# Optimization experiments

Measured on AMD Instinct MI355X. Metric: run time of the kernel, lower is better.

The kernel has to match this reference:

```python
import jax, jax.numpy as jnp
import numpy as np
import math

FANO_LINES = [(0,1,2),(0,3,4),(0,6,5),(1,3,5),(1,4,6),(2,3,6),(2,5,4)]
WINDOW = 16

def fano_mask(T: int) -> jnp.ndarray:
    """[7,T,T] bool mask: head h attends to j if (j%7 in line_h and j<=i) or i-WINDOW<=j<=i."""
    membership = np.zeros((7, 7), dtype=bool)
    for h, line in enumerate(FANO_LINES):
        membership[h, list(line)] = True
    j = np.arange(T)
    fano = membership[:, j % 7]                      # [7,T]
    i = j[:, None]
    causal = (j[None, :] <= i)                       # [T,T]
    local = causal & (j[None, :] >= i - WINDOW)      # [T,T]
    mask = (fano[:, None, :] & causal[None]) | local[None]
    return jnp.asarray(mask)

def setup_inputs() -> dict:
    key = jax.random.key(0)
    ks = jax.random.split(key, 5)
    B, T, D = 1, 4096, 896
    s = 1.0 / math.sqrt(D)
    return {
        "x":  jax.random.normal(ks[0], (B, T, D), dtype=jnp.float32),
        "Wq": jax.random.normal(ks[1], (D, D), dtype=jnp.float32) * s,
        "Wk": jax.random.normal(ks[2], (D, D), dtype=jnp.float32) * s,
        "Wv": jax.random.normal(ks[3], (D, D), dtype=jnp.float32) * s,
        "Wo": jax.random.normal(ks[4], (D, D), dtype=jnp.float32) * s,
    }

def reference(x, Wq, Wk, Wv, Wo):
    B, T, D = x.shape
    H = 7
    hd = D // H
    # torch Linear: x @ W.T
    q = (x @ Wq.T).reshape(B, T, H, hd)
    k = (x @ Wk.T).reshape(B, T, H, hd)
    v = (x @ Wv.T).reshape(B, T, H, hd)
    scale = 1.0 / math.sqrt(hd)
    scores = jnp.einsum('bthc,bshc->bhts', q, k) * scale   # [B,7,T,T]
    mask = fano_mask(T)                                    # [7,T,T]
    neg = jnp.asarray(-jnp.inf, dtype=scores.dtype)
    scores = jnp.where(mask[None], scores, neg)
    attn = jax.nn.softmax(scores, axis=-1)
    out = jnp.einsum('bhts,bshc->bthc', attn, v).reshape(B, T, D)
    return out @ Wo.T
```

## Files before the change

### kernel.cpp

```cpp
#include <hip/hip_runtime.h>
#include <stdint.h>

typedef unsigned short ushort_t;
typedef __bf16 bf16x8 __attribute__((ext_vector_type(8)));
typedef float f32x4 __attribute__((ext_vector_type(4)));

#define T_SEQ 4096
#define D_MODEL 896
#define NSPLIT 4

#define LSK 136
#define LSV 72
#define LSP 72

__constant__ int d_LINEMASK[7] = {0x07, 0x19, 0x61, 0x2A, 0x52, 0x4C, 0x34};
__constant__ int d_R[7][3] = {{0,1,2},{0,3,4},{0,5,6},{1,3,5},{1,4,6},{2,3,6},{2,4,5}};

__device__ inline unsigned f2bf(float f) {
    unsigned x = __float_as_uint(f);
    return (x + 0x7fffu + ((x >> 16) & 1u)) >> 16;
}
__device__ inline float lo_f(unsigned x) { return __uint_as_float(x << 16); }
__device__ inline float hi_f(unsigned x) { return __uint_as_float(x & 0xFFFF0000u); }

__global__ __launch_bounds__(256)
void cvt5(const float* __restrict__ x,  const float* __restrict__ wq,
          const float* __restrict__ wk, const float* __restrict__ wv,
          const float* __restrict__ wo,
          ushort_t* __restrict__ xb,  ushort_t* __restrict__ wqb,
          ushort_t* __restrict__ wkb, ushort_t* __restrict__ wvb,
          ushort_t* __restrict__ wob) {
    const int ten = blockIdx.y;
    const float* s = (ten == 0) ? x : (ten == 1) ? wq : (ten == 2) ? wk
                   : (ten == 3) ? wv : wo;
    ushort_t* d = (ten == 0) ? xb : (ten == 1) ? wqb : (ten == 2) ? wkb
                : (ten == 3) ? wvb : wob;
    const int n8 = ((ten == 0) ? T_SEQ * D_MODEL : D_MODEL * D_MODEL) >> 3;
    for (int i = blockIdx.x * 256 + threadIdx.x; i < n8; i += gridDim.x * 256) {
        float4 a = ((const float4*)s)[2 * i];
        float4 b = ((const float4*)s)[2 * i + 1];
        uint4 u;
        u.x = f2bf(a.x) | (f2bf(a.y) << 16);
        u.y = f2bf(a.z) | (f2bf(a.w) << 16);
        u.z = f2bf(b.x) | (f2bf(b.y) << 16);
        u.w = f2bf(b.z) | (f2bf(b.w) << 16);
        ((uint4*)d)[i] = u;
    }
}

__device__ __forceinline__ void async_cp16(const void* g, void* l) {
    __builtin_amdgcn_global_load_lds(
        (__attribute__((address_space(1))) void*)g,
        (__attribute__((address_space(3))) void*)l,
        16, 0, 0);
}

template <bool C32>
__global__ __launch_bounds__(256)
void gemm_nt_dma(const ushort_t* __restrict__ A,
                 const ushort_t* __restrict__ B0,
                 const ushort_t* __restrict__ B1,
                 const ushort_t* __restrict__ B2,
                 void* __restrict__ C0,
                 void* __restrict__ C1,
                 void* __restrict__ C2) {
    const int z = blockIdx.z;
    const ushort_t* B = (z == 0) ? B0 : (z == 1) ? B1 : B2;
    void* C = (z == 0) ? C0 : (z == 1) ? C1 : C2;

    const int K = D_MODEL, N = D_MODEL;
    const int i0 = blockIdx.x * 128;
    const int n0 = blockIdx.y * 128;

    __shared__ __align__(16) ushort_t As[128 * 32];
    __shared__ __align__(16) ushort_t Bs[128 * 32];

    const int t = threadIdx.x;
    const int w = t >> 6, lane = t & 63;
    const int wm = (w >> 1) * 64, wn = (w & 1) * 64;
    const int lr = lane & 15, lq = lane >> 4;

    const int srow = w * 16 + (lane >> 2);
    const int scol = (lane & 3) * 8;
    const ushort_t* gA0 = A + (size_t)(i0 + srow) * K + scol;
    const ushort_t* gA1 = A + (size_t)(i0 + 64 + srow) * K + scol;
    const ushort_t* gB0 = B + (size_t)(n0 + srow) * K + scol;
    const ushort_t* gB1 = B + (size_t)(n0 + 64 + srow) * K + scol;
    ushort_t* lA0 = &As[(w * 16) * 32];
    ushort_t* lA1 = &As[(64 + w * 16) * 32];
    ushort_t* lB0 = &Bs[(w * 16) * 32];
    ushort_t* lB1 = &Bs[(64 + w * 16) * 32];

    f32x4 acc[4][4];
#pragma unroll
    for (int a = 0; a < 4; a++)
#pragma unroll
        for (int b = 0; b < 4; b++) acc[a][b] = (f32x4){0.f, 0.f, 0.f, 0.f};

    for (int k0 = 0; k0 < K; k0 += 32) {
        __syncthreads();
        async_cp16(gA0 + k0, lA0);
        async_cp16(gA1 + k0, lA1);
        async_cp16(gB0 + k0, lB0);
        async_cp16(gB1 + k0, lB1);
        __builtin_amdgcn_s_waitcnt(0);
        __syncthreads();

        bf16x8 af[4], bfr[4];
#pragma unroll
        for (int mi = 0; mi < 4; mi++)
            af[mi] = *(const bf16x8*)&As[(wm + mi * 16 + lr) * 32 + lq * 8];
#pragma unroll
        for (int ni = 0; ni < 4; ni++)
            bfr[ni] = *(const bf16x8*)&Bs[(wn + ni * 16 + lr) * 32 + lq * 8];
#pragma unroll
        for (int mi = 0; mi < 4; mi++)
#pragma unroll
            for (int ni = 0; ni < 4; ni++)
                acc[mi][ni] = __builtin_amdgcn_mfma_f32_16x16x32_bf16(
                    af[mi], bfr[ni], acc[mi][ni], 0, 0, 0);
    }

    if (C32) {
        float* Cf = (float*)C;
#pragma unroll
        for (int mi = 0; mi < 4; mi++)
#pragma unroll
            for (int ni = 0; ni < 4; ni++)
#pragma unroll
                for (int r = 0; r < 4; r++) {
                    int row = i0 + wm + mi * 16 + lq * 4 + r;
                    int col = n0 + wn + ni * 16 + lr;
                    Cf[(size_t)row * N + col] = acc[mi][ni][r];
                }
    } else {
        ushort_t* Cb = (ushort_t*)C;
#pragma unroll
        for (int mi = 0; mi < 4; mi++)
#pragma unroll
            for (int ni = 0; ni < 4; ni++)
#pragma unroll
                for (int r = 0; r < 4; r++) {
                    int row = i0 + wm + mi * 16 + lq * 4 + r;
                    int col = n0 + wn + ni * 16 + lr;
                    Cb[(size_t)row * N + col] = (ushort_t)f2bf(acc[mi][ni][r]);
                }
    }
}

__device__ inline void vt_scatter8(ushort_t* vtcol, uint4 vv) {
    vtcol[0 * LSV] = (ushort_t)(vv.x & 0xFFFFu);
    vtcol[1 * LSV] = (ushort_t)(vv.x >> 16);
    vtcol[2 * LSV] = (ushort_t)(vv.y & 0xFFFFu);
    vtcol[3 * LSV] = (ushort_t)(vv.y >> 16);
    vtcol[4 * LSV] = (ushort_t)(vv.z & 0xFFFFu);
    vtcol[5 * LSV] = (ushort_t)(vv.z >> 16);
    vtcol[6 * LSV] = (ushort_t)(vv.w & 0xFFFFu);
    vtcol[7 * LSV] = (ushort_t)(vv.w >> 16);
}

__device__ inline int jof(int p, int r0, int r1, int r2) {
    int g = p / 3, rs = p - 3 * g;
    return 7 * g + ((rs == 0) ? r0 : (rs == 1) ? r1 : r2);
}

__device__ __forceinline__ void issue_kv(const ushort_t* __restrict__ Kb,
                                         const ushort_t* __restrict__ Vb,
                                         int j, int h, int dim0,
                                         uint4 kreg[4], uint4 vreg[4]) {
    if (j >= 0 && j < T_SEQ) {
        const ushort_t* kp = Kb + (size_t)j * D_MODEL + h * 128 + dim0;
        const ushort_t* vp = Vb + (size_t)j * D_MODEL + h * 128 + dim0;
#pragma unroll
        for (int v = 0; v < 4; v++) {
            kreg[v] = *(const uint4*)(kp + v * 8);
            vreg[v] = *(const uint4*)(vp + v * 8);
        }
    } else {
        uint4 zz = {0u, 0u, 0u, 0u};
#pragma unroll
        for (int v = 0; v < 4; v++) { kreg[v] = zz; vreg[v] = zz; }
    }
}

__device__ __forceinline__ void write_kv(ushort_t* Ks, ushort_t* Vt,
                                         int kk, int dim0,
                                         const uint4 kreg[4], const uint4 vreg[4]) {
#pragma unroll
    for (int v = 0; v < 4; v++) {
        *(uint4*)&Ks[kk * LSK + dim0 + v * 8] = kreg[v];
        vt_scatter8(&Vt[(dim0 + v * 8) * LSV + kk], vreg[v]);
    }
}

__global__ __launch_bounds__(256, 3)
void fano_attn_split(const ushort_t* __restrict__ Qb,
                     const ushort_t* __restrict__ Kb,
                     const ushort_t* __restrict__ Vb,
                     ushort_t* __restrict__ Opart,
                     float* __restrict__ Lm) {
    const int h = blockIdx.y;
    const int sp = blockIdx.z;
    const int tile = (int)gridDim.x - 1 - (int)blockIdx.x;
    const int i0 = tile * 64;
    const int t = threadIdx.x;
    const int w = t >> 6, lane = t & 63;
    const int lr = lane & 15, quad = lane >> 4;
    const int iw0 = i0 + w * 16;

    __shared__ __align__(16) ushort_t Ks[64 * LSK];
    __shared__ __align__(16) ushort_t Vt[128 * LSV];
    __shared__ __align__(16) ushort_t Ps[64 * LSP];

    const int lm = d_LINEMASK[h];
    const int r0 = d_R[h][0], r1 = d_R[h][1], r2 = d_R[h][2];
    const float scale = 0.08838834764831845f;

    bf16x8 qf[4];
    {
        const ushort_t* qrow = Qb + (size_t)(iw0 + lr) * D_MODEL + h * 128;
#pragma unroll
        for (int f = 0; f < 4; f++)
            qf[f] = *(const bf16x8*)(qrow + f * 32 + quad * 8);
    }

    f32x4 O[8];
#pragma unroll
    for (int dt = 0; dt < 8; dt++) O[dt] = (f32x4){0.f, 0.f, 0.f, 0.f};
    float m[4] = {-1e30f, -1e30f, -1e30f, -1e30f};
    float l[4] = {0.f, 0.f, 0.f, 0.f};

    const int imax = i0 + 63;
    const int ncomp = (imax - r0) / 7 + (imax - r1) / 7 + (imax - r2) / 7 + 3;
    const int nch = (ncomp + 63) >> 6;
    const int ntot = nch + 2;
    const int cstart = (sp * ntot) / NSPLIT;
    const int cend = ((sp + 1) * ntot) / NSPLIT;

    auto chunk_j = [&](int cc) -> int {
        if (cc >= nch) {
            const int jbase = (cc == nch) ? i0 - 16 : i0 + 48;
            return jbase + lane;
        }
        return jof(cc * 64 + lane, r0, r1, r2);
    };

    uint4 kreg[4], vreg[4];
    if (cstart < cend)
        issue_kv(Kb, Vb, chunk_j(cstart), h, w * 32, kreg, vreg);

    for (int cc = cstart; cc < cend; cc++) {
        const bool band = (cc >= nch);
        const int jbase = (cc == nch) ? i0 - 16 : i0 + 48;

        __syncthreads();
        write_kv(Ks, Vt, lane, w * 32, kreg, vreg);
        __syncthreads();

        if (cc + 1 < cend)
            issue_kv(Kb, Vb, chunk_j(cc + 1), h, w * 32, kreg, vreg);

        {
            int jmin = band ? jbase : jof(cc * 64, r0, r1, r2);
            if (jmin > iw0 + 15) continue;
        }

        f32x4 S[4];
#pragma unroll
        for (int tn = 0; tn < 4; tn++) S[tn] = (f32x4){0.f, 0.f, 0.f, 0.f};
#pragma unroll
        for (int f = 0; f < 4; f++) {
            bf16x8 kf[4];
#pragma unroll
            for (int tn = 0; tn < 4; tn++)
                kf[tn] = *(const bf16x8*)&Ks[(tn * 16 + lr) * LSK + f * 32 + quad * 8];
#pragma unroll
            for (int tn = 0; tn < 4; tn++)
                S[tn] = __builtin_amdgcn_mfma_f32_16x16x32_bf16(qf[f], kf[tn], S[tn], 0, 0, 0);
        }

#pragma unroll
        for (int tn = 0; tn < 4; tn++) {
            int j;
            bool okl = true;
            if (band) {
                j = jbase + tn * 16 + lr;
                int jm = ((j % 7) + 7) % 7;
                okl = (j >= 0) && !((lm >> jm) & 1);
            } else {
                j = jof(cc * 64 + tn * 16 + lr, r0, r1, r2);
            }
#pragma unroll
            for (int r = 0; r < 4; r++) {
                int ir = iw0 + quad * 4 + r;
                bool ok = okl && (j <= ir) && (!band || j >= ir - 16);
                S[tn][r] = ok ? S[tn][r] * scale : -1e30f;
            }
        }

        float a4[4], pvv[4][4];
#pragma unroll
        for (int r = 0; r < 4; r++) {
            float cm = fmaxf(fmaxf(S[0][r], S[1][r]), fmaxf(S[2][r], S[3][r]));
            cm = fmaxf(cm, __shfl_xor(cm, 1));
            cm = fmaxf(cm, __shfl_xor(cm, 2));
            cm = fmaxf(cm, __shfl_xor(cm, 4));
            cm = fmaxf(cm, __shfl_xor(cm, 8));
            float mn = fmaxf(fmaxf(m[r], cm), -60.f);
            a4[r] = __expf(m[r] - mn);
            m[r] = mn;
            float rs_ = 0.f;
#pragma unroll
            for (int tn = 0; tn < 4; tn++) {
                pvv[tn][r] = __expf(S[tn][r] - mn);
                rs_ += pvv[tn][r];
            }
            rs_ += __shfl_xor(rs_, 1);
            rs_ += __shfl_xor(rs_, 2);
            rs_ += __shfl_xor(rs_, 4);
            rs_ += __shfl_xor(rs_, 8);
            l[r] = l[r] * a4[r] + rs_;
            ushort_t* pp = &Ps[(w * 16 + quad * 4 + r) * LSP + lr];
            pp[0]  = (ushort_t)f2bf(pvv[0][r]);
            pp[16] = (ushort_t)f2bf(pvv[1][r]);
            pp[32] = (ushort_t)f2bf(pvv[2][r]);
            pp[48] = (ushort_t)f2bf(pvv[3][r]);
        }
#pragma unroll
        for (int dt = 0; dt < 8; dt++)
#pragma unroll
            for (int r = 0; r < 4; r++) O[dt][r] *= a4[r];

        bf16x8 pf0 = *(const bf16x8*)&Ps[(w * 16 + lr) * LSP + quad * 8];
        bf16x8 pf1 = *(const bf16x8*)&Ps[(w * 16 + lr) * LSP + 32 + quad * 8];
#pragma unroll
        for (int dt = 0; dt < 8; dt++) {
            bf16x8 v0 = *(const bf16x8*)&Vt[(dt * 16 + lr) * LSV + quad * 8];
            bf16x8 v1 = *(const bf16x8*)&Vt[(dt * 16 + lr) * LSV + 32 + quad * 8];
            O[dt] = __builtin_amdgcn_mfma_f32_16x16x32_bf16(pf0, v0, O[dt], 0, 0, 0);
            O[dt] = __builtin_amdgcn_mfma_f32_16x16x32_bf16(pf1, v1, O[dt], 0, 0, 0);
        }
    }

    const size_t pbase = ((size_t)sp * 7 + h) * T_SEQ;
#pragma unroll
    for (int dt = 0; dt < 8; dt++)
#pragma unroll
        for (int r = 0; r < 4; r++) {
            int row = iw0 + quad * 4 + r;
            Opart[(pbase + row) * 128 + dt * 16 + lr] = (ushort_t)f2bf(O[dt][r]);
        }
    if (lr == 0) {
#pragma unroll
        for (int r = 0; r < 4; r++) {
            int row = iw0 + quad * 4 + r;
            Lm[(pbase + row) * 2 + 0] = m[r];
            Lm[(pbase + row) * 2 + 1] = l[r];
        }
    }
}

__global__ __launch_bounds__(256)
void attn_merge(const ushort_t* __restrict__ Opart,
                const float* __restrict__ Lm,
                ushort_t* __restrict__ Ab) {
    const int h = blockIdx.y;
    const int row = blockIdx.x * 64 + (threadIdx.x >> 2);
    const int d0 = (threadIdx.x & 3) * 32;

    float ms[NSPLIT], ls[NSPLIT], M = -1e30f;
#pragma unroll
    for (int s = 0; s < NSPLIT; s++) {
        size_t pb = (((size_t)s * 7 + h) * T_SEQ + row) * 2;
        ms[s] = Lm[pb];
        ls[s] = Lm[pb + 1];
        M = fmaxf(M, ms[s]);
    }
    float L = 0.f, c[NSPLIT];
#pragma unroll
    for (int s = 0; s < NSPLIT; s++) {
        c[s] = __expf(ms[s] - M);
        L += c[s] * ls[s];
    }
    float acc[32];
#pragma unroll
    for (int k = 0; k < 32; k++) acc[k] = 0.f;
#pragma unroll
    for (int s = 0; s < NSPLIT; s++) {
        const ushort_t* op = Opart + (((size_t)s * 7 + h) * T_SEQ + row) * 128 + d0;
#pragma unroll
        for (int v = 0; v < 4; v++) {
            uint4 u = *(const uint4*)(op + v * 8);
            acc[v * 8 + 0] += c[s] * lo_f(u.x);
            acc[v * 8 + 1] += c[s] * hi_f(u.x);
            acc[v * 8 + 2] += c[s] * lo_f(u.y);
            acc[v * 8 + 3] += c[s] * hi_f(u.y);
            acc[v * 8 + 4] += c[s] * lo_f(u.z);
            acc[v * 8 + 5] += c[s] * hi_f(u.z);
            acc[v * 8 + 6] += c[s] * lo_f(u.w);
            acc[v * 8 + 7] += c[s] * hi_f(u.w);
        }
    }
    float invL = 1.f / L;
    ushort_t* dst = Ab + (size_t)row * D_MODEL + h * 128 + d0;
#pragma unroll
    for (int v = 0; v < 4; v++) {
        uint4 u;
        u.x = f2bf(acc[v * 8 + 0] * invL) | (f2bf(acc[v * 8 + 1] * invL) << 16);
        u.y = f2bf(acc[v * 8 + 2] * invL) | (f2bf(acc[v * 8 + 3] * invL) << 16);
        u.z = f2bf(acc[v * 8 + 4] * invL) | (f2bf(acc[v * 8 + 5] * invL) << 16);
        u.w = f2bf(acc[v * 8 + 6] * invL) | (f2bf(acc[v * 8 + 7] * invL) << 16);
        *(uint4*)(dst + v * 8) = u;
    }
}

extern "C" void kernel_launch(void* const* d_in, const int* in_sizes, int n_in,
                              void* d_out, int out_size, void* d_ws, size_t ws_size,
                              hipStream_t stream) {
    const float* x  = (const float*)d_in[0];
    const float* Wq = (const float*)d_in[1];
    const float* Wk = (const float*)d_in[2];
    const float* Wv = (const float*)d_in[3];
    const float* Wo = (const float*)d_in[4];

    const size_t n  = (size_t)T_SEQ * D_MODEL;
    const size_t nw = (size_t)D_MODEL * D_MODEL;
    ushort_t* xb  = (ushort_t*)d_ws + 128;
    ushort_t* Wqb = xb + n;
    ushort_t* Wkb = Wqb + nw;
    ushort_t* Wvb = Wkb + nw;
    ushort_t* Wob = Wvb + nw;
    ushort_t* Qb  = Wob + nw;
    ushort_t* Kb  = Qb + n;
    ushort_t* Vb  = Kb + n;
    ushort_t* Ab  = Vb + n;
    ushort_t* Opart = Ab + n;
    float*    Lm  = (float*)(Opart + (size_t)NSPLIT * 7 * T_SEQ * 128);

    cvt5<<<dim3(1792, 5), 256, 0, stream>>>(x, Wq, Wk, Wv, Wo,
                                            xb, Wqb, Wkb, Wvb, Wob);
    gemm_nt_dma<false><<<dim3(32, 7, 3), 256, 0, stream>>>(
        xb, Wqb, Wkb, Wvb, Qb, Kb, Vb);
    fano_attn_split<<<dim3(64, 7, NSPLIT), 256, 0, stream>>>(
        Qb, Kb, Vb, Opart, Lm);
    attn_merge<<<dim3(64, 7), 256, 0, stream>>>(Opart, Lm, Ab);
    gemm_nt_dma<true><<<dim3(32, 7, 1), 256, 0, stream>>>(
        Ab, Wob, Wob, Wob, d_out, d_out, d_out);
}
```

Baseline: 150.3 us.

## Use variable per-tile split-K count to balance fano attention work

New measurement: 139.0 us. -7.6%, faster.

```diff
diff --git a/kernel.cpp b/kernel.cpp
--- a/kernel.cpp
+++ b/kernel.cpp
@@ -7,7 +7,8 @@
 
 #define T_SEQ 4096
 #define D_MODEL 896
-#define NSPLIT 4
+#define CHUNKS_PER_BLOCK 4
+#define MAXSPLIT 8
 
 #define LSK 136
 #define LSV 72
@@ -22,6 +23,12 @@
 }
 __device__ inline float lo_f(unsigned x) { return __uint_as_float(x << 16); }
 __device__ inline float hi_f(unsigned x) { return __uint_as_float(x & 0xFFFF0000u); }
+
+__host__ __device__ inline int nsplit_of(int t) {
+    int a = (192 * t + 189) / 7 + 3;
+    int nch_ub = (a + 63) >> 6;
+    return (nch_ub + 2 + CHUNKS_PER_BLOCK - 1) / CHUNKS_PER_BLOCK;
+}
 
 __global__ __launch_bounds__(256)
 void cvt5(const float* __restrict__ x,  const float* __restrict__ wq,
@@ -200,8 +207,17 @@
                      ushort_t* __restrict__ Opart,
                      float* __restrict__ Lm) {
     const int h = blockIdx.y;
-    const int sp = blockIdx.z;
-    const int tile = (int)gridDim.x - 1 - (int)blockIdx.x;
+    const int p = (int)gridDim.x - 1 - (int)blockIdx.x;
+
+    int tile = 63, pbase0 = 0;
+    for (int u = 0; u < 64; ++u) {
+        int s = nsplit_of(u);
+        if (p < pbase0 + s) { tile = u; break; }
+        pbase0 += s;
+    }
+    const int sp = p - pbase0;
+    const int Sloc = nsplit_of(tile);
+
     const int i0 = tile * 64;
     const int t = threadIdx.x;
     const int w = t >> 6, lane = t & 63;
@@ -234,8 +250,8 @@
     const int ncomp = (imax - r0) / 7 + (imax - r1) / 7 + (imax - r2) / 7 + 3;
     const int nch = (ncomp + 63) >> 6;
     const int ntot = nch + 2;
-    const int cstart = (sp * ntot) / NSPLIT;
-    const int cend = ((sp + 1) * ntot) / NSPLIT;
+    const int cstart = (sp * ntot) / Sloc;
+    const int cend = ((sp + 1) * ntot) / Sloc;
 
     auto chunk_j = [&](int cc) -> int {
         if (cc >= nch) {
@@ -342,20 +358,20 @@
         }
     }
 
-    const size_t pbase = ((size_t)sp * 7 + h) * T_SEQ;
+    const size_t pbase = ((size_t)p * 7 + h) * 64;
 #pragma unroll
     for (int dt = 0; dt < 8; dt++)
 #pragma unroll
         for (int r = 0; r < 4; r++) {
-            int row = iw0 + quad * 4 + r;
-            Opart[(pbase + row) * 128 + dt * 16 + lr] = (ushort_t)f2bf(O[dt][r]);
+            int lrow = w * 16 + quad * 4 + r;
+            Opart[(pbase + lrow) * 128 + dt * 16 + lr] = (ushort_t)f2bf(O[dt][r]);
         }
     if (lr == 0) {
 #pragma unroll
         for (int r = 0; r < 4; r++) {
-            int row = iw0 + quad * 4 + r;
-            Lm[(pbase + row) * 2 + 0] = m[r];
-            Lm[(pbase + row) * 2 + 1] = l[r];
+            int lrow = w * 16 + quad * 4 + r;
+            Lm[(pbase + lrow) * 2 + 0] = m[r];
+            Lm[(pbase + lrow) * 2 + 1] = l[r];
         }
     }
 }
@@ -365,20 +381,29 @@
                 const float* __restrict__ Lm,
                 ushort_t* __restrict__ Ab) {
     const int h = blockIdx.y;
-    const int row = blockIdx.x * 64 + (threadIdx.x >> 2);
+    const int tt = blockIdx.x;
+    int pb = 0;
+    for (int u = 0; u < tt; ++u) pb += nsplit_of(u);
+    const int S = nsplit_of(tt);
+    const int lrow = threadIdx.x >> 2;
+    const int row = tt * 64 + lrow;
     const int d0 = (threadIdx.x & 3) * 32;
 
-    float ms[NSPLIT], ls[NSPLIT], M = -1e30f;
-#pragma unroll
-    for (int s = 0; s < NSPLIT; s++) {
-        size_t pb = (((size_t)s * 7 + h) * T_SEQ + row) * 2;
-        ms[s] = Lm[pb];
-        ls[s] = Lm[pb + 1];
+    float ms[MAXSPLIT], ls[MAXSPLIT], M = -1e30f;
+#pragma unroll
+    for (int s = 0; s < MAXSPLIT; s++) {
+        ms[s] = -1e30f;
+        ls[s] = 0.f;
+        if (s < S) {
+            size_t q = (((size_t)(pb + s) * 7 + h) * 64 + lrow) * 2;
+            ms[s] = Lm[q];
+            ls[s] = Lm[q + 1];
+        }
         M = fmaxf(M, ms[s]);
     }
-    float L = 0.f, c[NSPLIT];
-#pragma unroll
-    for (int s = 0; s < NSPLIT; s++) {
+    float L = 0.f, c[MAXSPLIT];
+#pragma unroll
+    for (int s = 0; s < MAXSPLIT; s++) {
         c[s] = __expf(ms[s] - M);
         L += c[s] * ls[s];
     }
@@ -386,19 +411,23 @@
 #pragma unroll
     for (int k = 0; k < 32; k++) acc[k] = 0.f;
 #pragma unroll
-    for (int s = 0; s < NSPLIT; s++) {
-        const ushort_t* op = Opart + (((size_t)s * 7 + h) * T_SEQ + row) * 128 + d0;
-#pragma unroll
-        for (int v = 0; v < 4; v++) {
-            uint4 u = *(const uint4*)(op + v * 8);
-            acc[v * 8 + 0] += c[s] * lo_f(u.x);
-            acc[v * 8 + 1] += c[s] * hi_f(u.x);
-            acc[v * 8 + 2] += c[s] * lo_f(u.y);
-            acc[v * 8 + 3] += c[s] * hi_f(u.y);
-            acc[v * 8 + 4] += c[s] * lo_f(u.z);
-            acc[v * 8 + 5] += c[s] * hi_f(u.z);
-            acc[v * 8 + 6] += c[s] * lo_f(u.w);
-            acc[v * 8 + 7] += c[s] * hi_f(u.w);
+    for (int s = 0; s < MAXSPLIT; s++) {
+        if (s < S) {
+            const float cs = c[s];
+            const ushort_t* op =
+                Opart + (((size_t)(pb + s) * 7 + h) * 64 + lrow) * 128 + d0;
+#pragma unroll
+            for (int v = 0; v < 4; v++) {
+                uint4 u = *(const uint4*)(op + v * 8);
+                acc[v * 8 + 0] += cs * lo_f(u.x);
+                acc[v * 8 + 1] += cs * hi_f(u.x);
+                acc[v * 8 + 2] += cs * lo_f(u.y);
+                acc[v * 8 + 3] += cs * hi_f(u.y);
+                acc[v * 8 + 4] += cs * lo_f(u.z);
+                acc[v * 8 + 5] += cs * hi_f(u.z);
+                acc[v * 8 + 6] += cs * lo_f(u.w);
+                acc[v * 8 + 7] += cs * hi_f(u.w);
+            }
         }
     }
     float invL = 1.f / L;
@@ -422,6 +451,9 @@
     const float* Wk = (const float*)d_in[2];
     const float* Wv = (const float*)d_in[3];
     const float* Wo = (const float*)d_in[4];
+
+    int NP = 0;
+    for (int u = 0; u < 64; ++u) NP += nsplit_of(u);
 
     const size_t n  = (size_t)T_SEQ * D_MODEL;
     const size_t nw = (size_t)D_MODEL * D_MODEL;
@@ -435,13 +467,13 @@
     ushort_t* Vb  = Kb + n;
     ushort_t* Ab  = Vb + n;
     ushort_t* Opart = Ab + n;
-    float*    Lm  = (float*)(Opart + (size_t)NSPLIT * 7 * T_SEQ * 128);
+    float*    Lm  = (float*)(Opart + (size_t)NP * 7 * 64 * 128);
 
     cvt5<<<dim3(1792, 5), 256, 0, stream>>>(x, Wq, Wk, Wv, Wo,
                                             xb, Wqb, Wkb, Wvb, Wob);
     gemm_nt_dma<false><<<dim3(32, 7, 3), 256, 0, stream>>>(
         xb, Wqb, Wkb, Wvb, Qb, Kb, Vb);
-    fano_attn_split<<<dim3(64, 7, NSPLIT), 256, 0, stream>>>(
+    fano_attn_split<<<dim3(NP, 7), 256, 0, stream>>>(
         Qb, Kb, Vb, Opart, Lm);
     attn_merge<<<dim3(64, 7), 256, 0, stream>>>(Opart, Lm, Ab);
     gemm_nt_dma<true><<<dim3(32, 7, 1), 256, 0, stream>>>(
```
